# Performance work log

Measured on AMD Instinct MI355X. Metric: run time of the kernel, lower is better.

Reference implementation:

```python
import jax, jax.numpy as jnp
import numpy as np

N_HEADS = 16
EMBED = 1024
HEAD_SIZE = 64
BLOCK = 2048
BATCH = 2
SEQ = 2048


def setup_inputs() -> dict:
    key = jax.random.key(0)
    ks = jax.random.split(key, 6)
    scale_e = 1.0 / np.sqrt(EMBED)
    x = jax.random.normal(ks[0], (BATCH, SEQ, EMBED), dtype=jnp.float32)
    # per-head Q/K/V projections (bias=False in nanoGPT-style SelfAttentionHead), stacked over heads
    wq = jax.random.normal(ks[1], (N_HEADS, EMBED, HEAD_SIZE), dtype=jnp.float32) * scale_e
    wk = jax.random.normal(ks[2], (N_HEADS, EMBED, HEAD_SIZE), dtype=jnp.float32) * scale_e
    wv = jax.random.normal(ks[3], (N_HEADS, EMBED, HEAD_SIZE), dtype=jnp.float32) * scale_e
    # output projection nn.Linear(embedding_size, embedding_size): y = x @ W^T + b
    w_proj = jax.random.normal(ks[4], (EMBED, EMBED), dtype=jnp.float32) * scale_e
    b_proj = jax.random.normal(ks[5], (EMBED,), dtype=jnp.float32) * 0.01
    return {"x": x, "wq": wq, "wk": wk, "wv": wv, "w_proj": w_proj, "b_proj": b_proj}


def reference(x, wq, wk, wv, w_proj, b_proj):
    B, S, E = x.shape
    # project all heads at once: [B, H, S, D]
    q = jnp.einsum('bse,hed->bhsd', x, wq)
    k = jnp.einsum('bse,hed->bhsd', x, wk)
    v = jnp.einsum('bse,hed->bhsd', x, wv)
    scale = 1.0 / jnp.sqrt(jnp.asarray(HEAD_SIZE, dtype=x.dtype))
    scores = jnp.einsum('bhqd,bhkd->bhqk', q, k) * scale  # [B,H,S,S]
    causal = jnp.tril(jnp.ones((S, S), dtype=bool))
    scores = jnp.where(causal, scores, -jnp.inf)
    attn = jax.nn.softmax(scores, axis=-1)  # (attn dropout inactive in eval)
    out = jnp.einsum('bhqk,bhkd->bhqd', attn, v)  # [B,H,S,D]
    # concat heads along last dim -> [B, S, H*D] == [B, S, E]
    out = out.transpose(0, 2, 1, 3).reshape(B, S, E)
    # output projection (dropout inactive in eval)
    return out @ w_proj.T + b_proj
```

## Files before the change

### kernel.cpp

```cpp
#include <hip/hip_runtime.h>
#include <hip/hip_bf16.h>


typedef __attribute__((ext_vector_type(4))) float  f32x4;
typedef __attribute__((ext_vector_type(8))) short  bf16x8;

#define S_LEN 2048
#define EMB   1024
#define NH    16
#define HD    64

#define LDSW 72

#define QSCALE 0.18033688011112042f

#if __has_builtin(__builtin_amdgcn_exp2f)
#define EXP2(x) __builtin_amdgcn_exp2f(x)
#else
#define EXP2(x) __exp2f(x)
#endif

__device__ __forceinline__ unsigned short f2bf(float f) {
    __hip_bfloat16 h = __float2bfloat16(f);
    return __builtin_bit_cast(unsigned short, h);
}
__device__ __forceinline__ unsigned int pk2bf(float a, float b) {
    unsigned int x = __builtin_bit_cast(unsigned int, a);
    unsigned int y = __builtin_bit_cast(unsigned int, b);
    x += 0x7FFFu + ((x >> 16) & 1u);
    y += 0x7FFFu + ((y >> 16) & 1u);
    return (x >> 16) | (y & 0xFFFF0000u);
}

__global__ __launch_bounds__(256) void prep(const float* __restrict__ x,
                                            const float* __restrict__ wq,
                                            const float* __restrict__ wk,
                                            const float* __restrict__ wv,
                                            const float* __restrict__ wproj,
                                            unsigned short* __restrict__ xb,
                                            unsigned short* __restrict__ wpb,
                                            unsigned short* __restrict__ wcat) {
    int blk = blockIdx.x;
    if (blk < 5120) {
        const float* in = (blk < 4096) ? x : wproj;
        unsigned short* out = (blk < 4096) ? xb : wpb;
        int bb = (blk < 4096) ? blk : blk - 4096;
        int i = (bb * 256 + threadIdx.x) * 4;
        float4 v = *(const float4*)(in + i);
        out[i + 0] = f2bf(v.x);
        out[i + 1] = f2bf(v.y);
        out[i + 2] = f2bf(v.z);
        out[i + 3] = f2bf(v.w);
    } else {
        int b2  = blk - 5120;
        int et  = b2 & 7;
        int h   = (b2 >> 3) & 15;
        int qkv = b2 >> 7;
        const float* w = (qkv == 0) ? wq : (qkv == 1) ? wk : wv;
        int t = threadIdx.x;
        int d = t & 63, es = t >> 6;
        int e0 = et * 128 + es * 32;

        unsigned short val[32];
        #pragma unroll
        for (int i = 0; i < 32; i++)
            val[i] = f2bf(w[(size_t)h * 65536 + (size_t)(e0 + i) * 64 + d]);

        size_t n = (size_t)qkv * 1024 + h * 64 + d;
        #pragma unroll
        for (int k = 0; k < 4; k++)
            *(uint4*)(wcat + n * 1024 + e0 + k * 8) = *(const uint4*)(val + k * 8);
    }
}

__device__ __forceinline__ void gemm_tile_core(const unsigned short* __restrict__ A,
                                               const unsigned short* __restrict__ Bt,
                                               int K, int m0, int n0,
                                               unsigned short* As, unsigned short* Bs,
                                               f32x4 acc[4][4]) {
    const int t    = threadIdx.x;
    const int wave = t >> 6, lane = t & 63;
    const int wm   = (wave >> 1) * 64, wn = (wave & 1) * 64;
    const int lr   = lane & 15, quad = lane >> 4;
    const int sr   = t >> 3;
    const int sc   = (t & 7) * 8;

    #pragma unroll
    for (int i = 0; i < 4; i++)
        #pragma unroll
        for (int j = 0; j < 4; j++) acc[i][j] = (f32x4)(0.0f);

    for (int k0 = 0; k0 < K; k0 += 64) {
        __syncthreads();
        #pragma unroll
        for (int p = 0; p < 4; ++p) {
            int r = p * 32 + sr;
            uint4 av = *(const uint4*)(A  + (size_t)(m0 + r) * K + k0 + sc);
            uint4 bv = *(const uint4*)(Bt + (size_t)(n0 + r) * K + k0 + sc);
            *(uint4*)(As + r * LDSW + sc) = av;
            *(uint4*)(Bs + r * LDSW + sc) = bv;
        }
        __syncthreads();
        #pragma unroll
        for (int kk = 0; kk < 64; kk += 32) {
            bf16x8 af[4], bfr[4];
            #pragma unroll
            for (int i = 0; i < 4; i++)
                af[i] = *(const bf16x8*)(As + (wm + i * 16 + lr) * LDSW + kk + quad * 8);
            #pragma unroll
            for (int j = 0; j < 4; j++)
                bfr[j] = *(const bf16x8*)(Bs + (wn + j * 16 + lr) * LDSW + kk + quad * 8);
            #pragma unroll
            for (int i = 0; i < 4; i++)
                #pragma unroll
                for (int j = 0; j < 4; j++)
                    acc[i][j] = __builtin_amdgcn_mfma_f32_16x16x32_bf16(af[i], bfr[j], acc[i][j], 0, 0, 0);
        }
    }
}

__global__ __launch_bounds__(256) void gemm_qkv(const unsigned short* __restrict__ xb,
                                                const unsigned short* __restrict__ wcat,
                                                unsigned short* __restrict__ qb,
                                                unsigned short* __restrict__ kb,
                                                unsigned short* __restrict__ vt) {
    __shared__ unsigned short Smem[2 * 128 * LDSW];
    unsigned short* As = Smem;
    unsigned short* Bs = Smem + 128 * LDSW;
    f32x4 acc[4][4];
    int m0 = blockIdx.x * 128, n0 = blockIdx.y * 128;
    gemm_tile_core(xb, wcat, EMB, m0, n0, As, Bs, acc);

    int t = threadIdx.x, wave = t >> 6, lane = t & 63;
    int wm = (wave >> 1) * 64, wn = (wave & 1) * 64, lr = lane & 15, quad = lane >> 4;
    int b  = m0 >> 11;
    int s0 = m0 & 2047;
    unsigned short* Tb = Smem;

    if (n0 < 2048) {
        bool isQ = (n0 < 1024);
        unsigned short* dst = isQ ? qb : kb;
        float sc = isQ ? QSCALE : 1.0f;
        __syncthreads();
        #pragma unroll
        for (int i = 0; i < 4; i++)
            #pragma unroll
            for (int j = 0; j < 4; j++)
                #pragma unroll
                for (int e = 0; e < 4; e++)
                    Tb[(wm + i * 16 + quad * 4 + e) * 136 + wn + j * 16 + lr] = f2bf(acc[i][j][e] * sc);
        __syncthreads();
        #pragma unroll
        for (int p = 0; p < 8; p++) {
            int r  = p * 16 + (t >> 4);
            int ch = (t & 15) * 8;
            int n  = n0 + ch;
            int h  = (n >> 6) & 15, d = ch & 63;
            *(uint4*)(dst + (((size_t)(b * NH + h)) * S_LEN + s0 + r) * HD + d) =
                *(const uint4*)(Tb + r * 136 + ch);
        }
    } else {
        __syncthreads();
        #pragma unroll
        for (int i = 0; i < 4; i++)
            #pragma unroll
            for (int j = 0; j < 4; j++)
                #pragma unroll
                for (int e = 0; e < 4; e++)
                    Tb[(wn + j * 16 + lr) * 136 + (wm + i * 16 + quad * 4 + e)] = f2bf(acc[i][j][e]);
        __syncthreads();
        #pragma unroll
        for (int p = 0; p < 8; p++) {
            int nl  = p * 16 + (t >> 4);
            int n   = n0 + nl;
            int h   = (n >> 6) & 15, d = n & 63;
            int col = (t & 15) * 8;
            *(uint4*)(vt + (((size_t)(b * NH + h)) * HD + d) * S_LEN + s0 + col) =
                *(const uint4*)(Tb + nl * 136 + col);
        }
    }
}

__global__ __launch_bounds__(256) void gemm_proj(const unsigned short* __restrict__ ao,
                                                 const unsigned short* __restrict__ wpb,
                                                 const float* __restrict__ bproj,
                                                 float* __restrict__ out) {
    __shared__ unsigned short Smem[2 * 128 * LDSW];
    f32x4 acc[4][4];
    int m0 = blockIdx.x * 128, n0 = blockIdx.y * 128;
    gemm_tile_core(ao, wpb, EMB, m0, n0, Smem, Smem + 128 * LDSW, acc);

    int t = threadIdx.x, wave = t >> 6, lane = t & 63;
    int wm = (wave >> 1) * 64, wn = (wave & 1) * 64, lr = lane & 15, quad = lane >> 4;
    #pragma unroll
    for (int i = 0; i < 4; i++)
        #pragma unroll
        for (int j = 0; j < 4; j++) {
            int n = n0 + wn + j * 16 + lr;
            float bias = bproj[n];
            #pragma unroll
            for (int e = 0; e < 4; e++) {
                int m = m0 + wm + i * 16 + quad * 4 + e;
                out[(size_t)m * EMB + n] = acc[i][j][e] + bias;
            }
        }
}

__global__ __launch_bounds__(512) void attn_mfma(const unsigned short* __restrict__ qb,
                                                 const unsigned short* __restrict__ kb,
                                                 const unsigned short* __restrict__ vtb,
                                                 unsigned short* __restrict__ ao) {
    __shared__ unsigned short Ks[2][64 * LDSW];
    __shared__ unsigned short Vs[2][64 * LDSW];
    __shared__ unsigned short Ps[128 * LDSW];

    int bIdx = blockIdx.x;
    int bh   = bIdx & 31;
    int grp  = bIdx >> 5;
    int chunk = (grp < 8) ? (15 - grp) : (grp - 8);
    int b = bh >> 4, h = bh & 15;
    int t = threadIdx.x, wave = t >> 6, lane = t & 63;
    int c = lane & 15, quad = lane >> 4;

    const unsigned short* Q  = qb  + (size_t)bh * S_LEN * HD;
    const unsigned short* K  = kb  + (size_t)bh * S_LEN * HD;
    const unsigned short* Vt = vtb + (size_t)bh * HD * S_LEN;

    int r0 = chunk * 128;
    int rw = r0 + wave * 16;

    bf16x8 Qf[2];
    #pragma unroll
    for (int ks = 0; ks < 2; ks++)
        Qf[ks] = *(const bf16x8*)(Q + (size_t)(rw + c) * HD + ks * 32 + quad * 8);

    f32x4 O[4];
    f32x4 lacc = (f32x4)(0.0f);
    #pragma unroll
    for (int dt = 0; dt < 4; dt++) O[dt] = (f32x4)(0.0f);

    const short oneb = (short)0x3F80;
    bf16x8 ones = {oneb, oneb, oneb, oneb, oneb, oneb, oneb, oneb};

    unsigned short* Pw = Ps + wave * 16 * LDSW;
    int sr = t >> 3, scg = (t & 7) * 8;

    int NT = (r0 + 128) >> 6;

    uint4 kpre = *(const uint4*)(K  + (size_t)sr * HD + scg);
    uint4 vpre = *(const uint4*)(Vt + (size_t)sr * S_LEN + scg);
    *(uint4*)(Ks[0] + sr * LDSW + scg) = kpre;
    *(uint4*)(Vs[0] + sr * LDSW + scg) = vpre;
    kpre = *(const uint4*)(K  + (size_t)(64 + sr) * HD + scg);
    vpre = *(const uint4*)(Vt + (size_t)sr * S_LEN + 64 + scg);

    for (int tt = 0; tt < NT; ++tt) {
        __syncthreads();
        if (tt + 1 < NT) {
            unsigned short* Kd = Ks[(tt + 1) & 1];
            unsigned short* Vd = Vs[(tt + 1) & 1];
            *(uint4*)(Kd + sr * LDSW + scg) = kpre;
            *(uint4*)(Vd + sr * LDSW + scg) = vpre;
            if (tt + 2 < NT) {
                kpre = *(const uint4*)(K  + (size_t)((tt + 2) * 64 + sr) * HD + scg);
                vpre = *(const uint4*)(Vt + (size_t)sr * S_LEN + (tt + 2) * 64 + scg);
            }
        }
        int j0 = tt << 6;
        if (j0 <= rw + 15) {
            const unsigned short* Kc = Ks[tt & 1];
            const unsigned short* Vc = Vs[tt & 1];

            f32x4 S4[4];
            #pragma unroll
            for (int kt = 0; kt < 4; kt++) S4[kt] = (f32x4)(0.0f);
            __builtin_amdgcn_s_setprio(1);
            #pragma unroll
            for (int ks = 0; ks < 2; ks++) {
                bf16x8 Kf[4];
                #pragma unroll
                for (int kt = 0; kt < 4; kt++)
                    Kf[kt] = *(const bf16x8*)(Kc + (kt * 16 + c) * LDSW + ks * 32 + quad * 8);
                #pragma unroll
                for (int kt = 0; kt < 4; kt++)
                    S4[kt] = __builtin_amdgcn_mfma_f32_16x16x32_bf16(Kf[kt], Qf[ks], S4[kt], 0, 0, 0);
            }
            __builtin_amdgcn_s_setprio(0);

            bool need_mask = (j0 + 63 > rw);
            #pragma unroll
            for (int kt = 0; kt < 4; kt++) {
                float p0 = EXP2(S4[kt][0]);
                float p1 = EXP2(S4[kt][1]);
                float p2 = EXP2(S4[kt][2]);
                float p3 = EXP2(S4[kt][3]);
                if (need_mask) {
                    int key  = j0 + kt * 16 + quad * 4;
                    int qrow = rw + c;
                    if (key + 0 > qrow) p0 = 0.0f;
                    if (key + 1 > qrow) p1 = 0.0f;
                    if (key + 2 > qrow) p2 = 0.0f;
                    if (key + 3 > qrow) p3 = 0.0f;
                }
                uint2 pk;
                pk.x = pk2bf(p0, p1);
                pk.y = pk2bf(p2, p3);
                *(uint2*)(Pw + c * LDSW + kt * 16 + quad * 4) = pk;
            }

            __builtin_amdgcn_s_setprio(1);
            #pragma unroll
            for (int ks = 0; ks < 2; ks++) {
                bf16x8 Af = *(const bf16x8*)(Pw + c * LDSW + ks * 32 + quad * 8);
                lacc = __builtin_amdgcn_mfma_f32_16x16x32_bf16(Af, ones, lacc, 0, 0, 0);
                #pragma unroll
                for (int dt = 0; dt < 4; dt++) {
                    bf16x8 Vf = *(const bf16x8*)(Vc + (dt * 16 + c) * LDSW + ks * 32 + quad * 8);
                    O[dt] = __builtin_amdgcn_mfma_f32_16x16x32_bf16(Af, Vf, O[dt], 0, 0, 0);
                }
            }
            __builtin_amdgcn_s_setprio(0);
        }
    }

    float inv[4];
    #pragma unroll
    for (int e = 0; e < 4; e++) inv[e] = 1.0f / lacc[e];

    #pragma unroll
    for (int dt = 0; dt < 4; dt++)
        #pragma unroll
        for (int e = 0; e < 4; e++)
            Ps[(wave * 16 + quad * 4 + e) * LDSW + dt * 16 + c] = f2bf(O[dt][e] * inv[e]);
    __syncthreads();
    #pragma unroll
    for (int p = 0; p < 2; p++) {
        int r = p * 64 + sr;
        *(uint4*)(ao + ((size_t)(b * S_LEN + r0 + r)) * EMB + h * HD + scg) =
            *(const uint4*)(Ps + r * LDSW + scg);
    }
}

extern "C" void kernel_launch(void* const* d_in, const int* in_sizes, int n_in,
                              void* d_out, int out_size, void* d_ws, size_t ws_size,
                              hipStream_t stream) {
    const float* x     = (const float*)d_in[0];
    const float* wq    = (const float*)d_in[1];
    const float* wk    = (const float*)d_in[2];
    const float* wv    = (const float*)d_in[3];
    const float* wproj = (const float*)d_in[4];
    const float* bproj = (const float*)d_in[5];
    float* out = (float*)d_out;

    char* ws = (char*)d_ws;
    unsigned short* xb   = (unsigned short*)(ws + 0);
    unsigned short* wcat = (unsigned short*)(ws + 8388608);
    unsigned short* wpb  = (unsigned short*)(ws + 14680064);
    unsigned short* qb   = (unsigned short*)(ws + 16777216);
    unsigned short* kb   = (unsigned short*)(ws + 25165824);
    unsigned short* vt   = (unsigned short*)(ws + 33554432);
    unsigned short* ao   = (unsigned short*)(ws + 41943040);

    prep<<<5504, 256, 0, stream>>>(x, wq, wk, wv, wproj, xb, wpb, wcat);
    gemm_qkv<<<dim3(32, 24), 256, 0, stream>>>(xb, wcat, qb, kb, vt);
    attn_mfma<<<512, 512, 0, stream>>>(qb, kb, vt, ao);
    gemm_proj<<<dim3(32, 8), 256, 0, stream>>>(ao, wpb, bproj, out);
}
```

Measured before the change: 180.1 us.

## Load K/V fragments directly from global memory and drop shared staging and barriers

The attention kernel no longer stages K and V tiles through double-buffered shared memory with block-wide barriers. Each wave now reads its MFMA operand fragments straight from global memory and runs only the number of key tiles its own rows need. This removes the per-tile __syncthreads and the LDS footprint, and adds a launch-bounds occupancy hint of 4 blocks. It also swaps the software bf16 rounding for the hardware packed convert instruction. The cost is redundant global and L2 traffic, since all eight waves load the same K/V, and no explicit prefetching to hide that latency.

Result: slower. 261.3 us (+45.1%).

```diff
diff --git a/kernel.cpp b/kernel.cpp
--- a/kernel.cpp
+++ b/kernel.cpp
@@ -30,6 +30,11 @@
     x += 0x7FFFu + ((x >> 16) & 1u);
     y += 0x7FFFu + ((y >> 16) & 1u);
     return (x >> 16) | (y & 0xFFFF0000u);
+}
+__device__ __forceinline__ unsigned int cvtpk(float lo, float hi) {
+    unsigned int r;
+    asm("v_cvt_pk_bf16_f32 %0, %1, %2" : "=v"(r) : "v"(lo), "v"(hi));
+    return r;
 }
 
 __global__ __launch_bounds__(256) void prep(const float* __restrict__ x,
@@ -206,12 +211,10 @@
         }
 }
 
-__global__ __launch_bounds__(512) void attn_mfma(const unsigned short* __restrict__ qb,
-                                                 const unsigned short* __restrict__ kb,
-                                                 const unsigned short* __restrict__ vtb,
-                                                 unsigned short* __restrict__ ao) {
-    __shared__ unsigned short Ks[2][64 * LDSW];
-    __shared__ unsigned short Vs[2][64 * LDSW];
+__global__ __launch_bounds__(512, 4) void attn_mfma(const unsigned short* __restrict__ qb,
+                                                    const unsigned short* __restrict__ kb,
+                                                    const unsigned short* __restrict__ vtb,
+                                                    unsigned short* __restrict__ ao) {
     __shared__ unsigned short Ps[128 * LDSW];
 
     int bIdx = blockIdx.x;
@@ -243,90 +246,71 @@
     bf16x8 ones = {oneb, oneb, oneb, oneb, oneb, oneb, oneb, oneb};
 
     unsigned short* Pw = Ps + wave * 16 * LDSW;
+
+    const unsigned short* Kfb = K  + (size_t)c * HD + quad * 8;
+    const unsigned short* Vfb = Vt + (size_t)c * S_LEN + quad * 8;
+
+    int ntw = ((rw + 15) >> 6) + 1;
+
+    for (int tt = 0; tt < ntw; ++tt) {
+        int j0 = tt << 6;
+
+        f32x4 S4[4];
+        #pragma unroll
+        for (int kt = 0; kt < 4; kt++) S4[kt] = (f32x4)(0.0f);
+        __builtin_amdgcn_s_setprio(1);
+        #pragma unroll
+        for (int ks = 0; ks < 2; ks++) {
+            bf16x8 Kf[4];
+            #pragma unroll
+            for (int kt = 0; kt < 4; kt++)
+                Kf[kt] = *(const bf16x8*)(Kfb + (size_t)(j0 + kt * 16) * HD + ks * 32);
+            #pragma unroll
+            for (int kt = 0; kt < 4; kt++)
+                S4[kt] = __builtin_amdgcn_mfma_f32_16x16x32_bf16(Kf[kt], Qf[ks], S4[kt], 0, 0, 0);
+        }
+        __builtin_amdgcn_s_setprio(0);
+
+        bool need_mask = (j0 + 63 > rw);
+        #pragma unroll
+        for (int kt = 0; kt < 4; kt++) {
+            float p0 = EXP2(S4[kt][0]);
+            float p1 = EXP2(S4[kt][1]);
+            float p2 = EXP2(S4[kt][2]);
+            float p3 = EXP2(S4[kt][3]);
+            if (need_mask) {
+                int key  = j0 + kt * 16 + quad * 4;
+                int qrow = rw + c;
+                if (key + 0 > qrow) p0 = 0.0f;
+                if (key + 1 > qrow) p1 = 0.0f;
+                if (key + 2 > qrow) p2 = 0.0f;
+                if (key + 3 > qrow) p3 = 0.0f;
+            }
+            uint2 pk;
+            pk.x = cvtpk(p0, p1);
+            pk.y = cvtpk(p2, p3);
+            *(uint2*)(Pw + c * LDSW + kt * 16 + quad * 4) = pk;
+        }
+
+        __builtin_amdgcn_s_setprio(1);
+        #pragma unroll
+        for (int ks = 0; ks < 2; ks++) {
+            bf16x8 Af = *(const bf16x8*)(Pw + c * LDSW + ks * 32 + quad * 8);
+            lacc = __builtin_amdgcn_mfma_f32_16x16x32_bf16(Af, ones, lacc, 0, 0, 0);
+            #pragma unroll
+            for (int dt = 0; dt < 4; dt++) {
+                bf16x8 Vf = *(const bf16x8*)(Vfb + (size_t)(dt * 16) * S_LEN + j0 + ks * 32);
+                O[dt] = __builtin_amdgcn_mfma_f32_16x16x32_bf16(Af, Vf, O[dt], 0, 0, 0);
+            }
+        }
+        __builtin_amdgcn_s_setprio(0);
+    }
+
+    float inv[4];
+    #pragma unroll
+    for (int e = 0; e < 4; e++) inv[e] = 1.0f / lacc[e];
+
     int sr = t >> 3, scg = (t & 7) * 8;
-
-    int NT = (r0 + 128) >> 6;
-
-    uint4 kpre = *(const uint4*)(K  + (size_t)sr * HD + scg);
-    uint4 vpre = *(const uint4*)(Vt + (size_t)sr * S_LEN + scg);
-    *(uint4*)(Ks[0] + sr * LDSW + scg) = kpre;
-    *(uint4*)(Vs[0] + sr * LDSW + scg) = vpre;
-    kpre = *(const uint4*)(K  + (size_t)(64 + sr) * HD + scg);
-    vpre = *(const uint4*)(Vt + (size_t)sr * S_LEN + 64 + scg);
-
-    for (int tt = 0; tt < NT; ++tt) {
-        __syncthreads();
-        if (tt + 1 < NT) {
-            unsigned short* Kd = Ks[(tt + 1) & 1];
-            unsigned short* Vd = Vs[(tt + 1) & 1];
-            *(uint4*)(Kd + sr * LDSW + scg) = kpre;
-            *(uint4*)(Vd + sr * LDSW + scg) = vpre;
-            if (tt + 2 < NT) {
-                kpre = *(const uint4*)(K  + (size_t)((tt + 2) * 64 + sr) * HD + scg);
-                vpre = *(const uint4*)(Vt + (size_t)sr * S_LEN + (tt + 2) * 64 + scg);
-            }
-        }
-        int j0 = tt << 6;
-        if (j0 <= rw + 15) {
-            const unsigned short* Kc = Ks[tt & 1];
-            const unsigned short* Vc = Vs[tt & 1];
-
-            f32x4 S4[4];
-            #pragma unroll
-            for (int kt = 0; kt < 4; kt++) S4[kt] = (f32x4)(0.0f);
-            __builtin_amdgcn_s_setprio(1);
-            #pragma unroll
-            for (int ks = 0; ks < 2; ks++) {
-                bf16x8 Kf[4];
-                #pragma unroll
-                for (int kt = 0; kt < 4; kt++)
-                    Kf[kt] = *(const bf16x8*)(Kc + (kt * 16 + c) * LDSW + ks * 32 + quad * 8);
-                #pragma unroll
-                for (int kt = 0; kt < 4; kt++)
-                    S4[kt] = __builtin_amdgcn_mfma_f32_16x16x32_bf16(Kf[kt], Qf[ks], S4[kt], 0, 0, 0);
-            }
-            __builtin_amdgcn_s_setprio(0);
-
-            bool need_mask = (j0 + 63 > rw);
-            #pragma unroll
-            for (int kt = 0; kt < 4; kt++) {
-                float p0 = EXP2(S4[kt][0]);
-                float p1 = EXP2(S4[kt][1]);
-                float p2 = EXP2(S4[kt][2]);
-                float p3 = EXP2(S4[kt][3]);
-                if (need_mask) {
-                    int key  = j0 + kt * 16 + quad * 4;
-                    int qrow = rw + c;
-                    if (key + 0 > qrow) p0 = 0.0f;
-                    if (key + 1 > qrow) p1 = 0.0f;
-                    if (key + 2 > qrow) p2 = 0.0f;
-                    if (key + 3 > qrow) p3 = 0.0f;
-                }
-                uint2 pk;
-                pk.x = pk2bf(p0, p1);
-                pk.y = pk2bf(p2, p3);
-                *(uint2*)(Pw + c * LDSW + kt * 16 + quad * 4) = pk;
-            }
-
-            __builtin_amdgcn_s_setprio(1);
-            #pragma unroll
-            for (int ks = 0; ks < 2; ks++) {
-                bf16x8 Af = *(const bf16x8*)(Pw + c * LDSW + ks * 32 + quad * 8);
-                lacc = __builtin_amdgcn_mfma_f32_16x16x32_bf16(Af, ones, lacc, 0, 0, 0);
-                #pragma unroll
-                for (int dt = 0; dt < 4; dt++) {
-                    bf16x8 Vf = *(const bf16x8*)(Vc + (dt * 16 + c) * LDSW + ks * 32 + quad * 8);
-                    O[dt] = __builtin_amdgcn_mfma_f32_16x16x32_bf16(Af, Vf, O[dt], 0, 0, 0);
-                }
-            }
-            __builtin_amdgcn_s_setprio(0);
-        }
-    }
-
-    float inv[4];
-    #pragma unroll
-    for (int e = 0; e < 4; e++) inv[e] = 1.0f / lacc[e];
-
     #pragma unroll
     for (int dt = 0; dt < 4; dt++)
         #pragma unroll
```

## Fuse fp32-to-bf16 conversion into GEMM loads and double-buffer LDS tiles

Applied to the files above, without the earlier changes.

Drops the separate conversion pass over x and w_proj. The QKV and projection GEMMs now read fp32 directly from global memory and convert with the hardware packed bf16 convert instruction, which saves a write and re-read of bf16 copies. The GEMM core gains a register-prefetched, double-buffered LDS pipeline with one barrier per K step, and the attention kernel uses the same hardware convert in place of software rounding. The trade-off is that the x tiles are loaded as fp32 and re-converted by each of the 24 column blocks, which doubles load bytes. LDS use also doubles, which may limit occupancy.

Result: slower. 268.8 us (+49.2%).

```diff
diff --git a/kernel.cpp b/kernel.cpp
--- a/kernel.cpp
+++ b/kernel.cpp
@@ -24,59 +24,41 @@
     __hip_bfloat16 h = __float2bfloat16(f);
     return __builtin_bit_cast(unsigned short, h);
 }
-__device__ __forceinline__ unsigned int pk2bf(float a, float b) {
-    unsigned int x = __builtin_bit_cast(unsigned int, a);
-    unsigned int y = __builtin_bit_cast(unsigned int, b);
-    x += 0x7FFFu + ((x >> 16) & 1u);
-    y += 0x7FFFu + ((y >> 16) & 1u);
-    return (x >> 16) | (y & 0xFFFF0000u);
-}
-
-__global__ __launch_bounds__(256) void prep(const float* __restrict__ x,
-                                            const float* __restrict__ wq,
-                                            const float* __restrict__ wk,
-                                            const float* __restrict__ wv,
-                                            const float* __restrict__ wproj,
-                                            unsigned short* __restrict__ xb,
-                                            unsigned short* __restrict__ wpb,
-                                            unsigned short* __restrict__ wcat) {
+__device__ __forceinline__ unsigned int cvtpk(float lo, float hi) {
+    unsigned int r;
+    asm("v_cvt_pk_bf16_f32 %0, %1, %2" : "=v"(r) : "v"(lo), "v"(hi));
+    return r;
+}
+
+__global__ __launch_bounds__(256) void prep_wcat(const float* __restrict__ wq,
+                                                 const float* __restrict__ wk,
+                                                 const float* __restrict__ wv,
+                                                 unsigned short* __restrict__ wcat) {
     int blk = blockIdx.x;
-    if (blk < 5120) {
-        const float* in = (blk < 4096) ? x : wproj;
-        unsigned short* out = (blk < 4096) ? xb : wpb;
-        int bb = (blk < 4096) ? blk : blk - 4096;
-        int i = (bb * 256 + threadIdx.x) * 4;
-        float4 v = *(const float4*)(in + i);
-        out[i + 0] = f2bf(v.x);
-        out[i + 1] = f2bf(v.y);
-        out[i + 2] = f2bf(v.z);
-        out[i + 3] = f2bf(v.w);
-    } else {
-        int b2  = blk - 5120;
-        int et  = b2 & 7;
-        int h   = (b2 >> 3) & 15;
-        int qkv = b2 >> 7;
-        const float* w = (qkv == 0) ? wq : (qkv == 1) ? wk : wv;
-        int t = threadIdx.x;
-        int d = t & 63, es = t >> 6;
-        int e0 = et * 128 + es * 32;
-
-        unsigned short val[32];
-        #pragma unroll
-        for (int i = 0; i < 32; i++)
-            val[i] = f2bf(w[(size_t)h * 65536 + (size_t)(e0 + i) * 64 + d]);
-
-        size_t n = (size_t)qkv * 1024 + h * 64 + d;
-        #pragma unroll
-        for (int k = 0; k < 4; k++)
-            *(uint4*)(wcat + n * 1024 + e0 + k * 8) = *(const uint4*)(val + k * 8);
-    }
-}
-
-__device__ __forceinline__ void gemm_tile_core(const unsigned short* __restrict__ A,
-                                               const unsigned short* __restrict__ Bt,
+    int et  = blk & 7;
+    int h   = (blk >> 3) & 15;
+    int qkv = blk >> 7;
+    const float* w = (qkv == 0) ? wq : (qkv == 1) ? wk : wv;
+    int t = threadIdx.x;
+    int d = t & 63, es = t >> 6;
+    int e0 = et * 128 + es * 32;
+
+    unsigned short val[32];
+    #pragma unroll
+    for (int i = 0; i < 32; i++)
+        val[i] = f2bf(w[(size_t)h * 65536 + (size_t)(e0 + i) * 64 + d]);
+
+    size_t n = (size_t)qkv * 1024 + h * 64 + d;
+    #pragma unroll
+    for (int k = 0; k < 4; k++)
+        *(uint4*)(wcat + n * 1024 + e0 + k * 8) = *(const uint4*)(val + k * 8);
+}
+
+template<int AF32, int BF32>
+__device__ __forceinline__ void gemm_tile_core(const void* __restrict__ Av,
+                                               const void* __restrict__ Btv,
                                                int K, int m0, int n0,
-                                               unsigned short* As, unsigned short* Bs,
+                                               unsigned short* S,
                                                f32x4 acc[4][4]) {
     const int t    = threadIdx.x;
     const int wave = t >> 6, lane = t & 63;
@@ -85,31 +67,68 @@
     const int sr   = t >> 3;
     const int sc   = (t & 7) * 8;
 
+    unsigned short* As[2] = { S,                 S + 2 * 128 * LDSW };
+    unsigned short* Bs[2] = { S + 128 * LDSW,    S + 3 * 128 * LDSW };
+
     #pragma unroll
     for (int i = 0; i < 4; i++)
         #pragma unroll
         for (int j = 0; j < 4; j++) acc[i][j] = (f32x4)(0.0f);
 
+    uint4 a[4], b[4];
+    #define GLOAD(k0)                                                              \
+        _Pragma("unroll")                                                          \
+        for (int p = 0; p < 4; ++p) {                                              \
+            int r = p * 32 + sr;                                                   \
+            if (AF32) {                                                            \
+                const float* Af = (const float*)Av + (size_t)(m0 + r) * K + (k0) + sc; \
+                float4 v0 = *(const float4*)Af;                                    \
+                float4 v1 = *(const float4*)(Af + 4);                              \
+                a[p].x = cvtpk(v0.x, v0.y); a[p].y = cvtpk(v0.z, v0.w);            \
+                a[p].z = cvtpk(v1.x, v1.y); a[p].w = cvtpk(v1.z, v1.w);            \
+            } else {                                                               \
+                a[p] = *(const uint4*)((const unsigned short*)Av + (size_t)(m0 + r) * K + (k0) + sc); \
+            }                                                                      \
+            if (BF32) {                                                            \
+                const float* Bf = (const float*)Btv + (size_t)(n0 + r) * K + (k0) + sc; \
+                float4 v0 = *(const float4*)Bf;                                    \
+                float4 v1 = *(const float4*)(Bf + 4);                              \
+                b[p].x = cvtpk(v0.x, v0.y); b[p].y = cvtpk(v0.z, v0.w);            \
+                b[p].z = cvtpk(v1.x, v1.y); b[p].w = cvtpk(v1.z, v1.w);            \
+            } else {                                                               \
+                b[p] = *(const uint4*)((const unsigned short*)Btv + (size_t)(n0 + r) * K + (k0) + sc); \
+            }                                                                      \
+        }
+    #define SSTORE(buf)                                                            \
+        _Pragma("unroll")                                                          \
+        for (int p = 0; p < 4; ++p) {                                              \
+            int r = p * 32 + sr;                                                   \
+            *(uint4*)(As[buf] + r * LDSW + sc) = a[p];                             \
+            *(uint4*)(Bs[buf] + r * LDSW + sc) = b[p];                             \
+        }
+
+    GLOAD(0);
+    SSTORE(0);
+    if (K > 64) { GLOAD(64); }
+
     for (int k0 = 0; k0 < K; k0 += 64) {
         __syncthreads();
-        #pragma unroll
-        for (int p = 0; p < 4; ++p) {
-            int r = p * 32 + sr;
-            uint4 av = *(const uint4*)(A  + (size_t)(m0 + r) * K + k0 + sc);
-            uint4 bv = *(const uint4*)(Bt + (size_t)(n0 + r) * K + k0 + sc);
-            *(uint4*)(As + r * LDSW + sc) = av;
-            *(uint4*)(Bs + r * LDSW + sc) = bv;
-        }
-        __syncthreads();
+        const int cur = (k0 >> 6) & 1;
+        if (k0 + 64 < K) {
+            SSTORE(cur ^ 1);
+            if (k0 + 128 < K) { GLOAD(k0 + 128); }
+        }
+        const unsigned short* Ac = As[cur];
+        const unsigned short* Bc = Bs[cur];
         #pragma unroll
         for (int kk = 0; kk < 64; kk += 32) {
             bf16x8 af[4], bfr[4];
             #pragma unroll
             for (int i = 0; i < 4; i++)
-                af[i] = *(const bf16x8*)(As + (wm + i * 16 + lr) * LDSW + kk + quad * 8);
+                af[i] = *(const bf16x8*)(Ac + (wm + i * 16 + lr) * LDSW + kk + quad * 8);
             #pragma unroll
             for (int j = 0; j < 4; j++)
-                bfr[j] = *(const bf16x8*)(Bs + (wn + j * 16 + lr) * LDSW + kk + quad * 8);
+                bfr[j] = *(const bf16x8*)(Bc + (wn + j * 16 + lr) * LDSW + kk + quad * 8);
             #pragma unroll
             for (int i = 0; i < 4; i++)
                 #pragma unroll
@@ -117,19 +136,19 @@
                     acc[i][j] = __builtin_amdgcn_mfma_f32_16x16x32_bf16(af[i], bfr[j], acc[i][j], 0, 0, 0);
         }
     }
-}
-
-__global__ __launch_bounds__(256) void gemm_qkv(const unsigned short* __restrict__ xb,
-                                                const unsigned short* __restrict__ wcat,
-                                                unsigned short* __restrict__ qb,
-                                                unsigned short* __restrict__ kb,
-                                                unsigned short* __restrict__ vt) {
-    __shared__ unsigned short Smem[2 * 128 * LDSW];
-    unsigned short* As = Smem;
-    unsigned short* Bs = Smem + 128 * LDSW;
+    #undef GLOAD
+    #undef SSTORE
+}
+
+__global__ __launch_bounds__(256, 2) void gemm_qkv(const float* __restrict__ x,
+                                                   const unsigned short* __restrict__ wcat,
+                                                   unsigned short* __restrict__ qb,
+                                                   unsigned short* __restrict__ kb,
+                                                   unsigned short* __restrict__ vt) {
+    __shared__ unsigned short Smem[4 * 128 * LDSW];
     f32x4 acc[4][4];
     int m0 = blockIdx.x * 128, n0 = blockIdx.y * 128;
-    gemm_tile_core(xb, wcat, EMB, m0, n0, As, Bs, acc);
+    gemm_tile_core<1, 0>(x, wcat, EMB, m0, n0, Smem, acc);
 
     int t = threadIdx.x, wave = t >> 6, lane = t & 63;
     int wm = (wave >> 1) * 64, wn = (wave & 1) * 64, lr = lane & 15, quad = lane >> 4;
@@ -181,14 +200,14 @@
     }
 }
 
-__global__ __launch_bounds__(256) void gemm_proj(const unsigned short* __restrict__ ao,
-                                                 const unsigned short* __restrict__ wpb,
-                                                 const float* __restrict__ bproj,
-                                                 float* __restrict__ out) {
-    __shared__ unsigned short Smem[2 * 128 * LDSW];
+__global__ __launch_bounds__(256, 2) void gemm_proj(const unsigned short* __restrict__ ao,
+                                                    const float* __restrict__ wproj,
+                                                    const float* __restrict__ bproj,
+                                                    float* __restrict__ out) {
+    __shared__ unsigned short Smem[4 * 128 * LDSW];
     f32x4 acc[4][4];
     int m0 = blockIdx.x * 128, n0 = blockIdx.y * 128;
-    gemm_tile_core(ao, wpb, EMB, m0, n0, Smem, Smem + 128 * LDSW, acc);
+    gemm_tile_core<0, 1>(ao, wproj, EMB, m0, n0, Smem, acc);
 
     int t = threadIdx.x, wave = t >> 6, lane = t & 63;
     int wm = (wave >> 1) * 64, wn = (wave & 1) * 64, lr = lane & 15, quad = lane >> 4;
@@ -303,8 +322,8 @@
                     if (key + 3 > qrow) p3 = 0.0f;
                 }
                 uint2 pk;
-                pk.x = pk2bf(p0, p1);
-                pk.y = pk2bf(p2, p3);
+                pk.x = cvtpk(p0, p1);
+                pk.y = cvtpk(p2, p3);
                 *(uint2*)(Pw + c * LDSW + kt * 16 + quad * 4) = pk;
             }
 
@@ -353,16 +372,14 @@
     float* out = (float*)d_out;
 
     char* ws = (char*)d_ws;
-    unsigned short* xb   = (unsigned short*)(ws + 0);
-    unsigned short* wcat = (unsigned short*)(ws + 8388608);
-    unsigned short* wpb  = (unsigned short*)(ws + 14680064);
-    unsigned short* qb   = (unsigned short*)(ws + 16777216);
-    unsigned short* kb   = (unsigned short*)(ws + 25165824);
-    unsigned short* vt   = (unsigned short*)(ws + 33554432);
-    unsigned short* ao   = (unsigned short*)(ws + 41943040);
-
-    prep<<<5504, 256, 0, stream>>>(x, wq, wk, wv, wproj, xb, wpb, wcat);
-    gemm_qkv<<<dim3(32, 24), 256, 0, stream>>>(xb, wcat, qb, kb, vt);
+    unsigned short* wcat = (unsigned short*)(ws + 0);
+    unsigned short* qb   = (unsigned short*)(ws + 8388608);
+    unsigned short* kb   = (unsigned short*)(ws + 16777216);
+    unsigned short* vt   = (unsigned short*)(ws + 25165824);
+    unsigned short* ao   = (unsigned short*)(ws + 33554432);
+
+    prep_wcat<<<384, 256, 0, stream>>>(wq, wk, wv, wcat);
+    gemm_qkv<<<dim3(32, 24), 256, 0, stream>>>(x, wcat, qb, kb, vt);
     attn_mfma<<<512, 512, 0, stream>>>(qb, kb, vt, ao);
-    gemm_proj<<<dim3(32, 8), 256, 0, stream>>>(ao, wpb, bproj, out);
-}
+    gemm_proj<<<dim3(32, 8), 256, 0, stream>>>(ao, wproj, bproj, out);
+}
```
